# Performance work log

Hardware: AMD Instinct MI355X
Metric: run time of the kernel (lower is better)

Reference implementation:

```python
import jax, jax.numpy as jnp
import numpy as np
import math

D = 1024
H = 16
S = 2048

def setup_inputs() -> dict:
    key = jax.random.key(0)
    k1, k2, k3 = jax.random.split(key, 3)
    x = jax.random.normal(k1, (2, S, D), dtype=jnp.float32)
    # nn.Linear(D, 3D): weight [3D, D], bias [3D]
    W = jax.random.normal(k2, (3 * D, D), dtype=jnp.float32) / math.sqrt(D)
    b = jax.random.normal(k3, (3 * D,), dtype=jnp.float32) * 0.01
    return {"x": x, "W": W, "b": b}

def reference(x, W, b):
    N, C, Dm = x.shape
    hd = Dm // H
    z = jnp.einsum('ncd,ed->nce', x, W) + b  # [N, C, 3D]
    k = z[:, :, :Dm].reshape(N, C, H, hd).transpose(0, 2, 1, 3)
    q = z[:, :, Dm:2 * Dm].reshape(N, C, H, hd).transpose(0, 2, 1, 3)
    v = z[:, :, 2 * Dm:].reshape(N, C, H, hd).transpose(0, 2, 1, 3)
    # NOTE: original scales by 1/sqrt(D) (full dim), not 1/sqrt(head_dim)
    scores = jnp.einsum('nhqd,nhkd->nhqk', q, k) / math.sqrt(Dm)
    causal = jnp.tril(jnp.ones((C, C), dtype=bool))
    scores = jnp.where(causal[None, None], scores, -jnp.inf)
    attn = jax.nn.softmax(scores, axis=-1)
    out = jnp.einsum('nhqk,nhkd->nhqd', attn, v)
    return out.transpose(0, 2, 1, 3).reshape(N, C, Dm)
```

## Files before the change

### kernel.cpp

```cpp
#include <hip/hip_runtime.h>
#include <hip/hip_bf16.h>

#define D_MODEL 1024
#define NH 16
#define HD 64
#define S_LEN 2048
#define NB 2
#define M_TOT 4096
#define N3 3072

typedef __attribute__((ext_vector_type(8))) short bf16x8;
typedef __attribute__((ext_vector_type(4))) float f32x4;
typedef __attribute__((ext_vector_type(4))) unsigned short u16x4;

__device__ __forceinline__ unsigned short f2bf(float f) {
    unsigned int u = __float_as_uint(f);
    u += 0x7fffu + ((u >> 16) & 1u);
    return (unsigned short)(u >> 16);
}
__device__ __forceinline__ float bf2f(unsigned short s) {
    return __uint_as_float((unsigned int)s << 16);
}

#define GLOAD_LDS(gp, lp)                                                      \
    __builtin_amdgcn_global_load_lds(                                          \
        (const __attribute__((address_space(1))) void*)(gp),                   \
        (__attribute__((address_space(3))) void*)(lp), 16, 0, 0)

__global__ __launch_bounds__(256) void cast_both(
    const float* __restrict__ x, const float* __restrict__ W,
    unsigned short* __restrict__ xb, unsigned short* __restrict__ Wb) {
    const int nx = M_TOT * D_MODEL / 4;
    const int nw = N3 * D_MODEL / 4;
    int i = blockIdx.x * 256 + threadIdx.x;
    const float* src;
    unsigned short* dst;
    int j;
    if (i < nx) { src = x; dst = xb; j = i; }
    else { j = i - nx; if (j >= nw) return; src = W; dst = Wb; }
    float4 v = reinterpret_cast<const float4*>(src)[j];
    u16x4 o;
    o.x = f2bf(v.x); o.y = f2bf(v.y); o.z = f2bf(v.z); o.w = f2bf(v.w);
    reinterpret_cast<u16x4*>(dst)[j] = o;
}

#define BM 128
#define BN 128
#define BK 64

__global__ __launch_bounds__(256) void qkv_gemm(
    const unsigned short* __restrict__ A, const unsigned short* __restrict__ B,
    const float* __restrict__ bias, unsigned short* __restrict__ Z) {
    __shared__ unsigned short As[BM * BK];
    __shared__ unsigned short Bs[BN * BK];

    const int t = threadIdx.x;
    const int lane = t & 63;
    const int wid = t >> 6;
    const int wr = wid >> 1, wc = wid & 1;
    const int bm = blockIdx.y, bn = blockIdx.x;
    const int lr = lane & 15;
    const int lg = lane >> 4;
    const int srow = lane >> 3;
    const int sslot = lane & 7;

    f32x4 acc[4][4] = {};

    for (int k0 = 0; k0 < 1024; k0 += BK) {
        __syncthreads();
#pragma unroll
        for (int p = 0; p < 4; ++p) {
            int rb = wid * 32 + p * 8;
            int row = rb + srow;
            int seg = sslot ^ (row & 7);
            GLOAD_LDS(&A[(size_t)(bm * BM + row) * 1024 + k0 + seg * 8],
                      &As[rb * BK]);
            GLOAD_LDS(&B[(size_t)(bn * BN + row) * 1024 + k0 + seg * 8],
                      &Bs[rb * BK]);
        }
        __syncthreads();
#pragma unroll
        for (int ks = 0; ks < 2; ++ks) {
            bf16x8 af[4], bfr[4];
#pragma unroll
            for (int m = 0; m < 4; ++m) {
                int row = wr * 64 + m * 16 + lr;
                int slot = (ks * 4 + lg) ^ (row & 7);
                af[m] = *reinterpret_cast<const bf16x8*>(&As[row * BK + slot * 8]);
            }
#pragma unroll
            for (int n = 0; n < 4; ++n) {
                int row = wc * 64 + n * 16 + lr;
                int slot = (ks * 4 + lg) ^ (row & 7);
                bfr[n] = *reinterpret_cast<const bf16x8*>(&Bs[row * BK + slot * 8]);
            }
#pragma unroll
            for (int m = 0; m < 4; ++m)
#pragma unroll
                for (int n = 0; n < 4; ++n)
                    acc[m][n] = __builtin_amdgcn_mfma_f32_16x16x32_bf16(
                        af[m], bfr[n], acc[m][n], 0, 0, 0);
        }
    }
#pragma unroll
    for (int m = 0; m < 4; ++m) {
        int row = bm * BM + wr * 64 + m * 16 + lg * 4;
#pragma unroll
        for (int n = 0; n < 4; ++n) {
            int col = bn * BN + wc * 64 + n * 16 + lr;
            float bv = bias[col];
#pragma unroll
            for (int i = 0; i < 4; ++i) {
                Z[(size_t)(row + i) * N3 + col] = f2bf(acc[m][n][i] + bv);
            }
        }
    }
}

__global__ __launch_bounds__(256) void transpose_v(
    const unsigned short* __restrict__ Z, unsigned short* __restrict__ Vt) {
    __shared__ unsigned short tile[64][72];
    int bid = blockIdx.x;
    int nh = bid >> 5;
    int cb = bid & 31;
    int n = nh >> 4, h = nh & 15;
    int t = threadIdx.x;
#pragma unroll
    for (int p = 0; p < 4; ++p) {
        int idx = p * 256 + t;
        int r = idx >> 4;
        int cg = idx & 15;
        u16x4 v = *reinterpret_cast<const u16x4*>(
            &Z[(size_t)(n * S_LEN + cb * 64 + r) * N3 + 2 * D_MODEL + h * HD + cg * 4]);
        *reinterpret_cast<u16x4*>(&tile[r][cg * 4]) = v;
    }
    __syncthreads();
#pragma unroll
    for (int p = 0; p < 4; ++p) {
        int idx = p * 256 + t;
        int d = idx >> 4;
        int cg = idx & 15;
        u16x4 o;
        o.x = tile[cg * 4 + 0][d];
        o.y = tile[cg * 4 + 1][d];
        o.z = tile[cg * 4 + 2][d];
        o.w = tile[cg * 4 + 3][d];
        *reinterpret_cast<u16x4*>(
            &Vt[((size_t)nh * 64 + d) * S_LEN + cb * 64 + cg * 4]) = o;
    }
}

__global__ __launch_bounds__(256) void attn(
    const unsigned short* __restrict__ Z, const unsigned short* __restrict__ Vt,
    float* __restrict__ Out) {
    const int ilin = blockIdx.y * 32 + blockIdx.x;
    const int head32 = (ilin & 7) * 4 + ((ilin >> 3) & 3);
    const int qb = 31 - (ilin >> 5);
    const int n = head32 >> 4, h = head32 & 15;

    __shared__ unsigned short Kt[2][64 * 64];
    __shared__ unsigned short Vs[2][64 * 64];
    __shared__ unsigned short p_lds[4][16][72];

    const int t = threadIdx.x;
    const int lane = t & 63, w = t >> 6;
    const int lr = lane & 15, lg = lane >> 4;
    const int srow = lane >> 3, sslot = lane & 7;

    const float SCL = 0.03125f * 1.44269504f;

    const size_t zrowQ = (size_t)(n * S_LEN + qb * 64 + w * 16 + lr) * N3 + D_MODEL + h * HD;
    bf16x8 qf[2];
#pragma unroll
    for (int f = 0; f < 2; ++f) {
        bf16x8 raw = *reinterpret_cast<const bf16x8*>(&Z[zrowQ + f * 32 + lg * 8]);
        bf16x8 sc;
#pragma unroll
        for (int j = 0; j < 8; ++j)
            sc[j] = (short)f2bf(bf2f((unsigned short)raw[j]) * SCL);
        qf[f] = sc;
    }

    auto STAGE = [&](int buf, int kb) {
#pragma unroll
        for (int p = 0; p < 2; ++p) {
            int rb = w * 16 + p * 8;
            int row = rb + srow;
            int seg = sslot ^ (row & 7);
            GLOAD_LDS(&Z[(size_t)(n * S_LEN + kb * 64 + row) * N3 + h * HD + seg * 8],
                      &Kt[buf][rb * 64]);
            GLOAD_LDS(&Vt[((size_t)head32 * 64 + row) * S_LEN + kb * 64 + seg * 8],
                      &Vs[buf][rb * 64]);
        }
    };

    f32x4 o[4] = {};
    float mrun = -1e30f, lrun = 0.f;

    STAGE(0, 0);
    int cur = 0;
    for (int kb = 0; kb <= qb; ++kb) {
        __syncthreads();
        if (kb < qb) STAGE(cur ^ 1, kb + 1);
        const unsigned short* Kc = &Kt[cur][0];
        const unsigned short* Vc = &Vs[cur][0];

        f32x4 s[4];
        __builtin_amdgcn_s_setprio(1);
#pragma unroll
        for (int cf = 0; cf < 4; ++cf) {
            int row = cf * 16 + lr;
            bf16x8 kf0 = *reinterpret_cast<const bf16x8*>(
                &Kc[row * 64 + ((lg) ^ (row & 7)) * 8]);
            bf16x8 kf1 = *reinterpret_cast<const bf16x8*>(
                &Kc[row * 64 + ((lg + 4) ^ (row & 7)) * 8]);
            f32x4 a = {};
            a = __builtin_amdgcn_mfma_f32_16x16x32_bf16(kf0, qf[0], a, 0, 0, 0);
            a = __builtin_amdgcn_mfma_f32_16x16x32_bf16(kf1, qf[1], a, 0, 0, 0);
            s[cf] = a;
        }
        __builtin_amdgcn_s_setprio(0);

        if (kb == qb) {
            const int qloc = w * 16 + lr;
#pragma unroll
            for (int cf = 0; cf < 4; ++cf) {
                int kbase = cf * 16 + lg * 4;
#pragma unroll
                for (int i = 0; i < 4; ++i)
                    if (kbase + i > qloc) s[cf][i] = -1e30f;
            }
        }

        float pm;
        {
            f32x4 m4 = s[0];
#pragma unroll
            for (int cf = 1; cf < 4; ++cf) {
                m4[0] = fmaxf(m4[0], s[cf][0]); m4[1] = fmaxf(m4[1], s[cf][1]);
                m4[2] = fmaxf(m4[2], s[cf][2]); m4[3] = fmaxf(m4[3], s[cf][3]);
            }
            pm = fmaxf(fmaxf(m4[0], m4[1]), fmaxf(m4[2], m4[3]));
            pm = fmaxf(pm, __shfl_xor(pm, 16));
            pm = fmaxf(pm, __shfl_xor(pm, 32));
        }
        if (!__all(pm - mrun <= 8.0f)) {
            float mn = fmaxf(mrun, pm);
            float corr = exp2f(mrun - mn);
            mrun = mn;
            lrun *= corr;
#pragma unroll
            for (int i = 0; i < 4; ++i) {
                float ci = __shfl(corr, lg * 4 + i);
#pragma unroll
                for (int cfd = 0; cfd < 4; ++cfd) o[cfd][i] *= ci;
            }
        }
        float sum = 0.f;
#pragma unroll
        for (int cf = 0; cf < 4; ++cf) {
#pragma unroll
            for (int i = 0; i < 4; ++i) {
                float p = exp2f(s[cf][i] - mrun);
                s[cf][i] = p;
                sum += p;
            }
            unsigned int lo01 = (unsigned int)f2bf(s[cf][0]) |
                                ((unsigned int)f2bf(s[cf][1]) << 16);
            unsigned int lo23 = (unsigned int)f2bf(s[cf][2]) |
                                ((unsigned int)f2bf(s[cf][3]) << 16);
            *reinterpret_cast<unsigned int*>(&p_lds[w][lr][cf * 16 + lg * 4]) = lo01;
            *reinterpret_cast<unsigned int*>(&p_lds[w][lr][cf * 16 + lg * 4 + 2]) = lo23;
        }
        sum += __shfl_xor(sum, 16);
        sum += __shfl_xor(sum, 32);
        lrun += sum;

        __builtin_amdgcn_s_setprio(1);
#pragma unroll
        for (int ks = 0; ks < 2; ++ks) {
            bf16x8 pf = *reinterpret_cast<const bf16x8*>(&p_lds[w][lr][ks * 32 + lg * 8]);
#pragma unroll
            for (int cfd = 0; cfd < 4; ++cfd) {
                int vrow = cfd * 16 + lr;
                bf16x8 vf = *reinterpret_cast<const bf16x8*>(
                    &Vc[vrow * 64 + ((ks * 4 + lg) ^ (vrow & 7)) * 8]);
                o[cfd] = __builtin_amdgcn_mfma_f32_16x16x32_bf16(pf, vf, o[cfd], 0, 0, 0);
            }
        }
        __builtin_amdgcn_s_setprio(0);
        cur ^= 1;
    }
#pragma unroll
    for (int i = 0; i < 4; ++i) {
        float li = __shfl(lrun, lg * 4 + i);
        float inv = 1.0f / li;
        int q = qb * 64 + w * 16 + lg * 4 + i;
#pragma unroll
        for (int cfd = 0; cfd < 4; ++cfd) {
            int d = h * HD + cfd * 16 + lr;
            Out[(size_t)(n * S_LEN + q) * D_MODEL + d] = o[cfd][i] * inv;
        }
    }
}

extern "C" void kernel_launch(void* const* d_in, const int* in_sizes, int n_in,
                              void* d_out, int out_size, void* d_ws, size_t ws_size,
                              hipStream_t stream) {
    const float* x = (const float*)d_in[0];
    const float* W = (const float*)d_in[1];
    const float* b = (const float*)d_in[2];
    float* out = (float*)d_out;

    char* ws = (char*)d_ws;
    unsigned short* xb = (unsigned short*)ws;
    unsigned short* Wb = (unsigned short*)(ws + (size_t)8 * 1024 * 1024);
    unsigned short* Z  = (unsigned short*)(ws + (size_t)14 * 1024 * 1024);
    unsigned short* Vt = (unsigned short*)(ws + (size_t)38 * 1024 * 1024);

    cast_both<<<7168, 256, 0, stream>>>(x, W, xb, Wb);
    qkv_gemm<<<dim3(N3 / BN, M_TOT / BM), 256, 0, stream>>>(xb, Wb, b, Z);
    transpose_v<<<1024, 256, 0, stream>>>(Z, Vt);
    attn<<<dim3(32, 32), 256, 0, stream>>>(Z, Vt, out);
}
```

Before: 173.3 us.

## Swap MFMA operands for row-major vector stores and load V directly to registers

The GEMM swaps its MFMA A/B operands so each lane holds four consecutive columns of one row, so the bias read and the bf16 Z store become 4-wide vector accesses instead of strided scalar stores. In attention the PV MFMA is transposed the same way, so each lane owns one query row: the softmax correction and final normalization no longer need per-row shuffles, and the output is written as float4. V tiles are no longer staged through LDS; each wave loads its V fragments straight from global memory into registers every iteration. This removes LDS traffic and halves attention LDS use, but adds per-wave global loads with no double buffering, which may stall on latency.

After: 194.9 us. 12.5% more time.

```diff
diff --git a/kernel.cpp b/kernel.cpp
--- a/kernel.cpp
+++ b/kernel.cpp
@@ -99,20 +99,22 @@
 #pragma unroll
                 for (int n = 0; n < 4; ++n)
                     acc[m][n] = __builtin_amdgcn_mfma_f32_16x16x32_bf16(
-                        af[m], bfr[n], acc[m][n], 0, 0, 0);
+                        bfr[n], af[m], acc[m][n], 0, 0, 0);
         }
     }
 #pragma unroll
     for (int m = 0; m < 4; ++m) {
-        int row = bm * BM + wr * 64 + m * 16 + lg * 4;
+        int row = bm * BM + wr * 64 + m * 16 + lr;
 #pragma unroll
         for (int n = 0; n < 4; ++n) {
-            int col = bn * BN + wc * 64 + n * 16 + lr;
-            float bv = bias[col];
-#pragma unroll
-            for (int i = 0; i < 4; ++i) {
-                Z[(size_t)(row + i) * N3 + col] = f2bf(acc[m][n][i] + bv);
-            }
+            int colb = bn * BN + wc * 64 + n * 16 + lg * 4;
+            float4 bv = *reinterpret_cast<const float4*>(&bias[colb]);
+            u16x4 pk;
+            pk.x = f2bf(acc[m][n][0] + bv.x);
+            pk.y = f2bf(acc[m][n][1] + bv.y);
+            pk.z = f2bf(acc[m][n][2] + bv.z);
+            pk.w = f2bf(acc[m][n][3] + bv.w);
+            *reinterpret_cast<u16x4*>(&Z[(size_t)row * N3 + colb]) = pk;
         }
     }
 }
@@ -159,7 +161,6 @@
     const int n = head32 >> 4, h = head32 & 15;
 
     __shared__ unsigned short Kt[2][64 * 64];
-    __shared__ unsigned short Vs[2][64 * 64];
     __shared__ unsigned short p_lds[4][16][72];
 
     const int t = threadIdx.x;
@@ -189,8 +190,6 @@
             int seg = sslot ^ (row & 7);
             GLOAD_LDS(&Z[(size_t)(n * S_LEN + kb * 64 + row) * N3 + h * HD + seg * 8],
                       &Kt[buf][rb * 64]);
-            GLOAD_LDS(&Vt[((size_t)head32 * 64 + row) * S_LEN + kb * 64 + seg * 8],
-                      &Vs[buf][rb * 64]);
         }
     };
 
@@ -203,7 +202,15 @@
         __syncthreads();
         if (kb < qb) STAGE(cur ^ 1, kb + 1);
         const unsigned short* Kc = &Kt[cur][0];
-        const unsigned short* Vc = &Vs[cur][0];
+
+        bf16x8 vf[2][4];
+#pragma unroll
+        for (int ks = 0; ks < 2; ++ks)
+#pragma unroll
+            for (int cfd = 0; cfd < 4; ++cfd)
+                vf[ks][cfd] = *reinterpret_cast<const bf16x8*>(
+                    &Vt[((size_t)head32 * 64 + cfd * 16 + lr) * S_LEN +
+                        kb * 64 + ks * 32 + lg * 8]);
 
         f32x4 s[4];
         __builtin_amdgcn_s_setprio(1);
@@ -250,11 +257,9 @@
             mrun = mn;
             lrun *= corr;
 #pragma unroll
-            for (int i = 0; i < 4; ++i) {
-                float ci = __shfl(corr, lg * 4 + i);
-#pragma unroll
-                for (int cfd = 0; cfd < 4; ++cfd) o[cfd][i] *= ci;
-            }
+            for (int cfd = 0; cfd < 4; ++cfd)
+#pragma unroll
+                for (int i = 0; i < 4; ++i) o[cfd][i] *= corr;
         }
         float sum = 0.f;
 #pragma unroll
@@ -282,24 +287,26 @@
             bf16x8 pf = *reinterpret_cast<const bf16x8*>(&p_lds[w][lr][ks * 32 + lg * 8]);
 #pragma unroll
             for (int cfd = 0; cfd < 4; ++cfd) {
-                int vrow = cfd * 16 + lr;
-                bf16x8 vf = *reinterpret_cast<const bf16x8*>(
-                    &Vc[vrow * 64 + ((ks * 4 + lg) ^ (vrow & 7)) * 8]);
-                o[cfd] = __builtin_amdgcn_mfma_f32_16x16x32_bf16(pf, vf, o[cfd], 0, 0, 0);
+                o[cfd] = __builtin_amdgcn_mfma_f32_16x16x32_bf16(
+                    vf[ks][cfd], pf, o[cfd], 0, 0, 0);
             }
         }
         __builtin_amdgcn_s_setprio(0);
         cur ^= 1;
     }
-#pragma unroll
-    for (int i = 0; i < 4; ++i) {
-        float li = __shfl(lrun, lg * 4 + i);
-        float inv = 1.0f / li;
-        int q = qb * 64 + w * 16 + lg * 4 + i;
+    {
+        float inv = 1.0f / lrun;
+        int q = qb * 64 + w * 16 + lr;
 #pragma unroll
         for (int cfd = 0; cfd < 4; ++cfd) {
-            int d = h * HD + cfd * 16 + lr;
-            Out[(size_t)(n * S_LEN + q) * D_MODEL + d] = o[cfd][i] * inv;
+            int dbase = h * HD + cfd * 16 + lg * 4;
+            float4 ov;
+            ov.x = o[cfd][0] * inv;
+            ov.y = o[cfd][1] * inv;
+            ov.z = o[cfd][2] * inv;
+            ov.w = o[cfd][3] * inv;
+            *reinterpret_cast<float4*>(
+                &Out[(size_t)(n * S_LEN + q) * D_MODEL + dbase]) = ov;
         }
     }
 }
```
